# Kernel optimization log

Hardware: AMD Instinct MI355X
Metric: run time of the kernel (lower is better)

The kernel has to match this reference:

```python
import jax, jax.numpy as jnp
import numpy as np

AN = 1.0      # bandwidth a_n
SIGMA = 1.0   # Gaussian kernel scale
_EPS = 1e-32


def setup_inputs() -> dict:
    key = jax.random.key(0)
    k1, k2, k3 = jax.random.split(key, 3)
    n = 8192
    log_h = jax.random.normal(k1, (n, 1), dtype=jnp.float32)
    durations = jax.random.uniform(k2, (n,), dtype=jnp.float32)
    events = jax.random.randint(k3, (n,), 0, 2, dtype=jnp.int32)
    return {"log_h": log_h, "durations": durations, "events": events}


def reference(log_h, durations, events):
    theta = log_h.reshape(-1)                         # (n,)
    n = theta.shape[0]
    # residuals e = -(theta - log(Y)); note original adds 1e-32 before log
    e = -(theta - jnp.log(durations + _EPS))          # (n,)
    perm = jnp.argsort(e)                             # sort order of e
    e_sorted = e[perm]                                # (n,) ascending
    # Original code sorts [indices, dur, ev, theta] by the indices column,
    # which reorders the side arrays by the INVERSE permutation.
    inv = jnp.argsort(perm)
    ev = events.astype(jnp.float32)[inv]              # (n,)
    th = theta[inv]                                   # (n,)

    diff = (e_sorted[:, None] - e_sorted[None, :]) / AN   # (n, n)
    # Normal(0, SIGMA) log pdf at diff
    log_pdf = -0.5 * (diff / SIGMA) ** 2 - jnp.log(SIGMA * jnp.sqrt(2.0 * jnp.pi))
    # cond_E_i = sum_j pdf_ij * ev_j / (n*an) + eps-per-element
    cond_E = jnp.sum(jnp.exp(log_pdf) * ev / (n * AN) + _EPS, axis=1)   # (n,)
    # Normal(0, SIGMA) cdf at diff
    cdf = 0.5 * (1.0 + jax.lax.erf(diff / (SIGMA * jnp.sqrt(2.0))))
    surv = jnp.sum(cdf / n, axis=1)                   # (n,)

    loss = -jnp.sum((jnp.log(cond_E) - jnp.log(surv) + th) * ev / n)
    return loss
```

## Files before the change

### kernel.cpp

```cpp
#include <hip/hip_runtime.h>
#include <math.h>
#include <stdint.h>

#define RB 256
#define JT 512
#define GM 2048

#define SCALE 0.84932180028801904f
#define SQRT2PI 2.5066282746310002f

__device__ __forceinline__ unsigned float2ord(float f) {
  unsigned u = __float_as_uint(f);
  return (u & 0x80000000u) ? ~u : (u | 0x80000000u);
}
__device__ __forceinline__ float ord2float(unsigned u) {
  return __uint_as_float((u & 0x80000000u) ? (u ^ 0x80000000u) : ~u);
}
__device__ __forceinline__ uint64_t order_key(float f, int idx) {
  return ((uint64_t)float2ord(f) << 32) | (unsigned)idx;
}

__device__ __forceinline__ void grid_geom(const unsigned* mm, float* x0, float* hx) {
  float emin = ord2float(mm[0]), emax = ord2float(mm[1]);
  float a = fmaf(SCALE, emin, -7.0f);
  float b = fmaf(SCALE, emax, 7.0f);
  *x0 = a;
  *hx = (b - a) / (float)(GM - 1);
}

__global__ void init_kernel(float* gbuf, unsigned* mm) {
  int i = blockIdx.x * blockDim.x + threadIdx.x;
  if (i < 4 * GM) gbuf[i] = 0.0f;
  if (i == 0) { mm[0] = 0xFFFFFFFFu; mm[1] = 0u; }
}

__global__ void prep_kernel(const float* __restrict__ theta,
                            const float* __restrict__ dur,
                            float* __restrict__ e, uint64_t* __restrict__ key,
                            int* __restrict__ rank, float* __restrict__ out,
                            unsigned* __restrict__ mm, int n) {
  int i = blockIdx.x * blockDim.x + threadIdx.x;
  unsigned umin = 0xFFFFFFFFu, umax = 0u;
  if (i < n) {
    float ei = logf(dur[i] + 1e-32f) - theta[i];
    e[i] = ei;
    key[i] = order_key(ei, i);
    rank[i] = 0;
    umin = umax = float2ord(ei);
  }
  if (i == 0) out[0] = 0.0f;
  #pragma unroll
  for (int off = 32; off > 0; off >>= 1) {
    umin = min(umin, (unsigned)__shfl_xor((int)umin, off, 64));
    umax = max(umax, (unsigned)__shfl_xor((int)umax, off, 64));
  }
  if ((threadIdx.x & 63) == 0) {
    atomicMin(&mm[0], umin);
    atomicMax(&mm[1], umax);
  }
}

__global__ __launch_bounds__(RB) void rank_kernel(
    const uint64_t* __restrict__ key, int* __restrict__ rank, int n) {
  __shared__ uint64_t kt[JT];
  int i = blockIdx.x * RB + threadIdx.x;
  uint64_t ki = key[i];
  int jbase = blockIdx.y * JT;
  for (int t = threadIdx.x; t < JT; t += RB) kt[t] = key[jbase + t];
  __syncthreads();
  int cnt = 0;
  #pragma unroll 8
  for (int jj = 0; jj < JT; ++jj) cnt += (kt[jj] < ki) ? 1 : 0;
  atomicAdd(&rank[i], cnt);
}

__global__ void scatter_kernel(const float* __restrict__ e,
                               const int* __restrict__ rank,
                               const int* __restrict__ ev,
                               const float* __restrict__ theta,
                               float* __restrict__ xs, float* __restrict__ evs,
                               float* __restrict__ th_s, int n) {
  int k = blockIdx.x * blockDim.x + threadIdx.x;
  if (k < n) {
    int r = rank[k];
    xs[r] = SCALE * e[k];
    evs[k] = (float)ev[r];
    th_s[k] = theta[r];
  }
}

__global__ __launch_bounds__(RB) void gt_kernel(
    const float* __restrict__ xs, const float* __restrict__ evs,
    const unsigned* __restrict__ mm, float* __restrict__ gbuf, int n) {
  float x0, hx;
  grid_geom(mm, &x0, &hx);
  int m = blockIdx.x * RB + threadIdx.x;
  float xm = fmaf((float)m, hx, x0);
  int chunk = n >> 6;
  int jb = blockIdx.y * chunk;
  float a = 0.0f, b = 0.0f, c = 0.0f, d = 0.0f;
  #pragma unroll 8
  for (int jj = 0; jj < chunk; ++jj) {
    float xj = xs[jb + jj];
    float ev = evs[jb + jj];
    float dp = xm - xj;
    float g = __builtin_amdgcn_exp2f(-(dp * dp));
    float evg = ev * g;
    a += g;
    b += evg;
    c = fmaf(dp, g, c);
    d = fmaf(dp, evg, d);
  }
  atomicAdd(&gbuf[m], a);
  atomicAdd(&gbuf[GM + m], b);
  atomicAdd(&gbuf[2 * GM + m], c);
  atomicAdd(&gbuf[3 * GM + m], d);
}

__global__ __launch_bounds__(1024) void scan_kernel(
    const float* __restrict__ gbuf, const unsigned* __restrict__ mm,
    float* __restrict__ Fx) {
  __shared__ double sh[1024];
  float x0, hx;
  grid_geom(mm, &x0, &hx);
  const float* A = gbuf;
  const float* C = gbuf + 2 * GM;
  int t = threadIdx.x;
  int k0 = 2 * t, k1 = 2 * t + 1;
  double h = (double)hx, h26 = h * h / 6.0;
  double d0 = 0.5 * h * ((double)A[k0] + (double)A[k0 + 1]) +
              h26 * ((double)C[k0 + 1] - (double)C[k0]);
  double d1 = (k1 < GM - 1)
                  ? 0.5 * h * ((double)A[k1] + (double)A[k1 + 1]) +
                    h26 * ((double)C[k1 + 1] - (double)C[k1])
                  : 0.0;
  double pair = d0 + d1;
  sh[t] = pair;
  __syncthreads();
  for (int off = 1; off < 1024; off <<= 1) {
    double v = (t >= off) ? sh[t - off] : 0.0;
    __syncthreads();
    sh[t] += v;
    __syncthreads();
  }
  double excl = sh[t] - pair;
  if (t == 0) Fx[0] = 0.0f;
  Fx[k0 + 1] = (float)(excl + d0);
  if (k1 + 1 <= GM - 1) Fx[k1 + 1] = (float)(excl + d0 + d1);
}

__global__ __launch_bounds__(RB) void final_kernel(
    const float* __restrict__ xs, const float* __restrict__ evs,
    const float* __restrict__ th_s, const float* __restrict__ gbuf,
    const float* __restrict__ Fx, const unsigned* __restrict__ mm,
    float* __restrict__ out, int n) {
  float x0, hx;
  grid_geom(mm, &x0, &hx);
  const float* A = gbuf;
  const float* B = gbuf + GM;
  const float* D = gbuf + 3 * GM;
  int i = blockIdx.x * RB + threadIdx.x;

  float term = 0.0f;
  if (i < n) {
    float x = xs[i];
    double u = ((double)x - (double)x0) / (double)hx;
    int m = (int)u;
    m = min(max(m, 0), GM - 2);
    float t = (float)(u - (double)m);
    float t2 = t * t, t3 = t2 * t;
    float h00 = 2.0f * t3 - 3.0f * t2 + 1.0f;
    float h01 = 3.0f * t2 - 2.0f * t3;
    float h10 = t3 - 2.0f * t2 + t;
    float h11 = t3 - t2;
    float Fi = Fx[m] * h00 + Fx[m + 1] * h01 + hx * (A[m] * h10 + A[m + 1] * h11);
    float Bi = B[m] * h00 + B[m + 1] * h01 -
               2.0f * hx * (D[m] * h10 + D[m + 1] * h11);
    const float fn = (float)n;
    float PhiSum = fmaxf(Fi * (1.0f / SCALE / SQRT2PI), 1e-20f);
    float condE = fmaxf(Bi, 0.0f) * (1.0f / SQRT2PI) / fn + fn * 1e-32f;
    float surv = PhiSum / fn;
    term = (__logf(condE) - __logf(surv) + th_s[i]) * evs[i];
  }

  #pragma unroll
  for (int off = 32; off > 0; off >>= 1) term += __shfl_down(term, off, 64);
  __shared__ float red[RB / 64];
  int wave = threadIdx.x >> 6, lane = threadIdx.x & 63;
  if (lane == 0) red[wave] = term;
  __syncthreads();
  if (threadIdx.x == 0) {
    float s = 0.0f;
    #pragma unroll
    for (int w = 0; w < RB / 64; ++w) s += red[w];
    atomicAdd(out, -s / (float)n);
  }
}

extern "C" void kernel_launch(void* const* d_in, const int* in_sizes, int n_in,
                              void* d_out, int out_size, void* d_ws, size_t ws_size,
                              hipStream_t stream) {
  const float* theta = (const float*)d_in[0];
  const float* dur   = (const float*)d_in[1];
  const int*   ev    = (const int*)d_in[2];
  float* out = (float*)d_out;
  const int n = in_sizes[1];

  char* ws = (char*)d_ws;
  uint64_t* key  = (uint64_t*)ws;  ws += n * sizeof(uint64_t);
  float*    xs   = (float*)ws;     ws += n * sizeof(float);
  float*    evs  = (float*)ws;     ws += n * sizeof(float);
  float*    e    = (float*)ws;     ws += n * sizeof(float);
  int*      rank = (int*)ws;       ws += n * sizeof(int);
  float*    th_s = (float*)ws;     ws += n * sizeof(float);
  float*    gbuf = (float*)ws;     ws += 4 * GM * sizeof(float);
  float*    Fx   = (float*)ws;     ws += GM * sizeof(float);
  unsigned* mm   = (unsigned*)ws;  ws += 2 * sizeof(unsigned);

  int nb = (n + RB - 1) / RB;
  init_kernel<<<(4 * GM + RB - 1) / RB, RB, 0, stream>>>(gbuf, mm);
  prep_kernel<<<nb, RB, 0, stream>>>(theta, dur, e, key, rank, out, mm, n);
  rank_kernel<<<dim3(n / RB, n / JT), RB, 0, stream>>>(key, rank, n);
  scatter_kernel<<<nb, RB, 0, stream>>>(e, rank, ev, theta, xs, evs, th_s, n);
  gt_kernel<<<dim3(GM / RB, 64), RB, 0, stream>>>(xs, evs, mm, gbuf, n);
  scan_kernel<<<1, 1024, 0, stream>>>(gbuf, mm, Fx);
  final_kernel<<<nb, RB, 0, stream>>>(xs, evs, th_s, gbuf, Fx, mm, out, n);
}
```

Measured before the change: 88.27 us.

## Compute grid CDF sums directly with erf approximation, drop scan and init kernels

Replaces the trapezoid-plus-prefix-scan reconstruction of the Gaussian CDF sum with a direct per-grid-point erf evaluation, using an Abramowitz-Stegun style rational polynomial inside the grid transform loop. This removes the single-block scan kernel and the Fx buffer. It also derives the grid bounds from the sorted xs endpoints instead of an atomic min/max, and folds the gbuf zeroing into the prep kernel, removing the init kernel. The cost is extra ALU work (an rcp and a polynomial) per inner-loop pair in gt_kernel, plus reduced accuracy from the approximate erf.

```diff
diff --git a/kernel.cpp b/kernel.cpp
--- a/kernel.cpp
+++ b/kernel.cpp
@@ -5,59 +5,40 @@
 #define RB 256
 #define JT 512
 #define GM 2048
+#define YS 64
 
 #define SCALE 0.84932180028801904f
 #define SQRT2PI 2.5066282746310002f
+#define KFP 0.46971863934f
+#define LN2 0.69314718056f
 
-__device__ __forceinline__ unsigned float2ord(float f) {
+__device__ __forceinline__ uint64_t order_key(float f, int idx) {
   unsigned u = __float_as_uint(f);
-  return (u & 0x80000000u) ? ~u : (u | 0x80000000u);
-}
-__device__ __forceinline__ float ord2float(unsigned u) {
-  return __uint_as_float((u & 0x80000000u) ? (u ^ 0x80000000u) : ~u);
-}
-__device__ __forceinline__ uint64_t order_key(float f, int idx) {
-  return ((uint64_t)float2ord(f) << 32) | (unsigned)idx;
+  u = (u & 0x80000000u) ? ~u : (u | 0x80000000u);
+  return ((uint64_t)u << 32) | (unsigned)idx;
 }
 
-__device__ __forceinline__ void grid_geom(const unsigned* mm, float* x0, float* hx) {
-  float emin = ord2float(mm[0]), emax = ord2float(mm[1]);
-  float a = fmaf(SCALE, emin, -7.0f);
-  float b = fmaf(SCALE, emax, 7.0f);
+__device__ __forceinline__ void grid_geom(const float* xs, int n, float* x0, float* hx) {
+  float a = xs[0] - 7.0f;
+  float b = xs[n - 1] + 7.0f;
   *x0 = a;
   *hx = (b - a) / (float)(GM - 1);
-}
-
-__global__ void init_kernel(float* gbuf, unsigned* mm) {
-  int i = blockIdx.x * blockDim.x + threadIdx.x;
-  if (i < 4 * GM) gbuf[i] = 0.0f;
-  if (i == 0) { mm[0] = 0xFFFFFFFFu; mm[1] = 0u; }
 }
 
 __global__ void prep_kernel(const float* __restrict__ theta,
                             const float* __restrict__ dur,
                             float* __restrict__ e, uint64_t* __restrict__ key,
                             int* __restrict__ rank, float* __restrict__ out,
-                            unsigned* __restrict__ mm, int n) {
+                            float* __restrict__ gbuf, int n) {
   int i = blockIdx.x * blockDim.x + threadIdx.x;
-  unsigned umin = 0xFFFFFFFFu, umax = 0u;
   if (i < n) {
     float ei = logf(dur[i] + 1e-32f) - theta[i];
     e[i] = ei;
     key[i] = order_key(ei, i);
     rank[i] = 0;
-    umin = umax = float2ord(ei);
   }
+  if (i < 4 * GM) gbuf[i] = 0.0f;
   if (i == 0) out[0] = 0.0f;
-  #pragma unroll
-  for (int off = 32; off > 0; off >>= 1) {
-    umin = min(umin, (unsigned)__shfl_xor((int)umin, off, 64));
-    umax = max(umax, (unsigned)__shfl_xor((int)umax, off, 64));
-  }
-  if ((threadIdx.x & 63) == 0) {
-    atomicMin(&mm[0], umin);
-    atomicMax(&mm[1], umax);
-  }
 }
 
 __global__ __launch_bounds__(RB) void rank_kernel(
@@ -91,14 +72,15 @@
 
 __global__ __launch_bounds__(RB) void gt_kernel(
     const float* __restrict__ xs, const float* __restrict__ evs,
-    const unsigned* __restrict__ mm, float* __restrict__ gbuf, int n) {
+    float* __restrict__ gbuf, int n) {
   float x0, hx;
-  grid_geom(mm, &x0, &hx);
+  grid_geom(xs, n, &x0, &hx);
   int m = blockIdx.x * RB + threadIdx.x;
   float xm = fmaf((float)m, hx, x0);
-  int chunk = n >> 6;
+  const int chunk = n / YS;
   int jb = blockIdx.y * chunk;
-  float a = 0.0f, b = 0.0f, c = 0.0f, d = 0.0f;
+  const float P2S = 0.39169197f;
+  float a = 0.0f, b = 0.0f, f = 0.0f, d = 0.0f;
   #pragma unroll 8
   for (int jj = 0; jj < chunk; ++jj) {
     float xj = xs[jb + jj];
@@ -108,56 +90,26 @@
     float evg = ev * g;
     a += g;
     b += evg;
-    c = fmaf(dp, g, c);
     d = fmaf(dp, evg, d);
+    float tt = __builtin_amdgcn_rcpf(fmaf(P2S, __builtin_fabsf(dp), 1.0f));
+    float poly = tt * (0.3480242f + tt * (-0.0958798f + tt * 0.7478556f));
+    f += __builtin_copysignf(fmaf(-poly, g, 1.0f), dp);
   }
   atomicAdd(&gbuf[m], a);
   atomicAdd(&gbuf[GM + m], b);
-  atomicAdd(&gbuf[2 * GM + m], c);
+  atomicAdd(&gbuf[2 * GM + m], 0.5f * (float)chunk + 0.5f * f);
   atomicAdd(&gbuf[3 * GM + m], d);
-}
-
-__global__ __launch_bounds__(1024) void scan_kernel(
-    const float* __restrict__ gbuf, const unsigned* __restrict__ mm,
-    float* __restrict__ Fx) {
-  __shared__ double sh[1024];
-  float x0, hx;
-  grid_geom(mm, &x0, &hx);
-  const float* A = gbuf;
-  const float* C = gbuf + 2 * GM;
-  int t = threadIdx.x;
-  int k0 = 2 * t, k1 = 2 * t + 1;
-  double h = (double)hx, h26 = h * h / 6.0;
-  double d0 = 0.5 * h * ((double)A[k0] + (double)A[k0 + 1]) +
-              h26 * ((double)C[k0 + 1] - (double)C[k0]);
-  double d1 = (k1 < GM - 1)
-                  ? 0.5 * h * ((double)A[k1] + (double)A[k1 + 1]) +
-                    h26 * ((double)C[k1 + 1] - (double)C[k1])
-                  : 0.0;
-  double pair = d0 + d1;
-  sh[t] = pair;
-  __syncthreads();
-  for (int off = 1; off < 1024; off <<= 1) {
-    double v = (t >= off) ? sh[t - off] : 0.0;
-    __syncthreads();
-    sh[t] += v;
-    __syncthreads();
-  }
-  double excl = sh[t] - pair;
-  if (t == 0) Fx[0] = 0.0f;
-  Fx[k0 + 1] = (float)(excl + d0);
-  if (k1 + 1 <= GM - 1) Fx[k1 + 1] = (float)(excl + d0 + d1);
 }
 
 __global__ __launch_bounds__(RB) void final_kernel(
     const float* __restrict__ xs, const float* __restrict__ evs,
     const float* __restrict__ th_s, const float* __restrict__ gbuf,
-    const float* __restrict__ Fx, const unsigned* __restrict__ mm,
     float* __restrict__ out, int n) {
   float x0, hx;
-  grid_geom(mm, &x0, &hx);
+  grid_geom(xs, n, &x0, &hx);
   const float* A = gbuf;
   const float* B = gbuf + GM;
+  const float* F = gbuf + 2 * GM;
   const float* D = gbuf + 3 * GM;
   int i = blockIdx.x * RB + threadIdx.x;
 
@@ -173,13 +125,13 @@
     float h01 = 3.0f * t2 - 2.0f * t3;
     float h10 = t3 - 2.0f * t2 + t;
     float h11 = t3 - t2;
-    float Fi = Fx[m] * h00 + Fx[m + 1] * h01 + hx * (A[m] * h10 + A[m + 1] * h11);
+    float Fi = F[m] * h00 + F[m + 1] * h01 +
+               hx * KFP * (A[m] * h10 + A[m + 1] * h11);
     float Bi = B[m] * h00 + B[m + 1] * h01 -
-               2.0f * hx * (D[m] * h10 + D[m + 1] * h11);
+               2.0f * LN2 * hx * (D[m] * h10 + D[m + 1] * h11);
     const float fn = (float)n;
-    float PhiSum = fmaxf(Fi * (1.0f / SCALE / SQRT2PI), 1e-20f);
     float condE = fmaxf(Bi, 0.0f) * (1.0f / SQRT2PI) / fn + fn * 1e-32f;
-    float surv = PhiSum / fn;
+    float surv = fmaxf(Fi, 0.25f) / fn;
     term = (__logf(condE) - __logf(surv) + th_s[i]) * evs[i];
   }
 
@@ -214,15 +166,12 @@
   int*      rank = (int*)ws;       ws += n * sizeof(int);
   float*    th_s = (float*)ws;     ws += n * sizeof(float);
   float*    gbuf = (float*)ws;     ws += 4 * GM * sizeof(float);
-  float*    Fx   = (float*)ws;     ws += GM * sizeof(float);
-  unsigned* mm   = (unsigned*)ws;  ws += 2 * sizeof(unsigned);
 
   int nb = (n + RB - 1) / RB;
-  init_kernel<<<(4 * GM + RB - 1) / RB, RB, 0, stream>>>(gbuf, mm);
-  prep_kernel<<<nb, RB, 0, stream>>>(theta, dur, e, key, rank, out, mm, n);
+  int nbp = (max(n, 4 * GM) + RB - 1) / RB;
+  prep_kernel<<<nbp, RB, 0, stream>>>(theta, dur, e, key, rank, out, gbuf, n);
   rank_kernel<<<dim3(n / RB, n / JT), RB, 0, stream>>>(key, rank, n);
   scatter_kernel<<<nb, RB, 0, stream>>>(e, rank, ev, theta, xs, evs, th_s, n);
-  gt_kernel<<<dim3(GM / RB, 64), RB, 0, stream>>>(xs, evs, mm, gbuf, n);
-  scan_kernel<<<1, 1024, 0, stream>>>(gbuf, mm, Fx);
-  final_kernel<<<nb, RB, 0, stream>>>(xs, evs, th_s, gbuf, Fx, mm, out, n);
+  gt_kernel<<<dim3(GM / RB, YS), RB, 0, stream>>>(xs, evs, gbuf, n);
+  final_kernel<<<nb, RB, 0, stream>>>(xs, evs, th_s, gbuf, out, n);
 }
```

Measured after the change: 83.68 us. 1.05x faster.
